# Performance work log

Measured on AMD Instinct MI355X. Metric: run time of the kernel, lower is better.

The kernel has to match this reference:

```python
import jax, jax.numpy as jnp
import numpy as np

EPS = 1e-8


def _conv3x3(x, w, b):
    # x: [B,Ci,H,W], w: [Co,Ci,3,3], 'SAME' padding (stride 1)
    y = jax.lax.conv_general_dilated(x, w, (1, 1), 'SAME',
        dimension_numbers=('NCHW', 'OIHW', 'NCHW'))
    return y + b[None, :, None, None]


def _box3(x):
    # depthwise 3x3 box-sum with zero padding (uniform-kernel masked conv)
    C = x.shape[1]
    k = jnp.ones((C, 1, 3, 3), x.dtype)
    return jax.lax.conv_general_dilated(x, k, (1, 1), 'SAME',
        dimension_numbers=('NCHW', 'OIHW', 'NCHW'), feature_group_count=C)


def _unfold3(x):
    # stack_channel(1,9,k=3,p=1): x [B,1,H,W] -> 9 shifted copies [B,9,H,W]
    H, W = x.shape[-2:]
    xp = jnp.pad(x, ((0, 0), (0, 0), (1, 1), (1, 1)))
    return jnp.concatenate([xp[:, :, i:i + H, j:j + W]
                            for i in range(3) for j in range(3)], axis=1)


def _entropy(x):
    # generate_entropy: sigmoid(neighbor - center) averaged over the 3x3 patch
    # x: [B,1,H,W] -> [B,H,W]
    return jax.nn.sigmoid(_unfold3(x) - x).mean(axis=1)


def _pwf(x, params):
    # PixelWeightedFusionSoftmax: 1x1-conv + ReLU chain 2C->128->32->8->1
    for w, b in params:
        x = jax.nn.relu(jnp.einsum('oc,bchw->bohw', w, x) + b[None, :, None, None])
    return x


def _forward(bevs, compress_w, compress_b, pwf_params):
    BT, N, C, H, W = bevs.shape
    tg = bevs[:, 0]                                    # ego agent  [BT,C,H,W]
    nb = bevs[:, 1:].reshape(BT * (N - 1), C, H, W)    # neighbors

    # myCompressNet: 64 -> 1 channel
    tg_com = jax.nn.relu(_conv3x3(tg, compress_w, compress_b))   # [BT,1,H,W]
    nb_com = jax.nn.relu(_conv3x3(nb, compress_w, compress_b))   # [BT*(N-1),1,H,W]

    tg_ent = _entropy(tg_com)                                    # [BT,H,W]
    nb_ent = _entropy(nb_com).reshape(BT, N - 1, H, W)

    # attention_collaboration: select pixels where neighbor entropy exceeds ego's
    mask = (nb_ent > tg_ent[:, None]).astype(bevs.dtype)         # [BT,N-1,H,W]
    bandwidth = mask.mean()                                      # count / (H*W), averaged

    # conv_mask_uniform / interplot_f: partial conv w/ uniform 3x3 kernel
    m = mask.reshape(BT * (N - 1), 1, H, W)
    num = _box3(nb * m)                                          # [BT*(N-1),C,H,W]
    den = _box3(m)
    inter = num / (den + EPS)
    warp = m * nb + (1.0 - m) * inter

    # all-zero neighbors (min+max==0) are passed through untouched
    is_zero = (nb.min(axis=(1, 2, 3)) + nb.max(axis=(1, 2, 3))) == 0
    warp = jnp.where(is_zero[:, None, None, None], nb, warp)

    feats = jnp.concatenate([tg[:, None], warp.reshape(BT, N - 1, C, H, W)],
                            axis=1)                              # [BT,N,C,H,W]

    # per-agent pixel weights: exp / sum-exp normalize, then weighted fusion
    cat = jnp.concatenate([jnp.broadcast_to(tg[:, None], feats.shape), feats],
                          axis=2)                                # [BT,N,2C,H,W]
    logits = _pwf(cat.reshape(BT * N, 2 * C, H, W), pwf_params)
    logits = logits.reshape(BT, N, 1, H, W)
    wts = jnp.exp(logits)
    wts = wts / wts.sum(axis=1, keepdims=True)
    fused = (wts * feats).sum(axis=1)                            # [BT,C,H,W]
    return fused, bandwidth


def setup_inputs() -> dict:
    key = jax.random.key(0)
    ks = jax.random.split(key, 6)
    BT, N, C, H, W = 3, 5, 64, 200, 200
    s = 0.05
    return {
        'bevs': jax.random.normal(ks[0], (BT, N, C, H, W), jnp.float32),
        'compress_w': jax.random.normal(ks[1], (1, C, 3, 3), jnp.float32) * s,
        'compress_b': jnp.zeros((1,), jnp.float32),
        'pwf_w1': jax.random.normal(ks[2], (128, 2 * C), jnp.float32) * s,
        'pwf_b1': jnp.zeros((128,), jnp.float32),
        'pwf_w2': jax.random.normal(ks[3], (32, 128), jnp.float32) * s,
        'pwf_b2': jnp.zeros((32,), jnp.float32),
        'pwf_w3': jax.random.normal(ks[4], (8, 32), jnp.float32) * s,
        'pwf_b3': jnp.zeros((8,), jnp.float32),
        'pwf_w4': jax.random.normal(ks[5], (1, 8), jnp.float32) * s,
        'pwf_b4': jnp.zeros((1,), jnp.float32),
    }


def reference(bevs, compress_w, compress_b, pwf_w1, pwf_b1, pwf_w2, pwf_b2,
              pwf_w3, pwf_b3, pwf_w4, pwf_b4):
    pwf = [(pwf_w1, pwf_b1), (pwf_w2, pwf_b2), (pwf_w3, pwf_b3), (pwf_w4, pwf_b4)]
    return _forward(bevs, compress_w, compress_b, pwf)
```

## Files before the change

kernel.cpp:

```cpp
#include <hip/hip_runtime.h>
#include <hip/hip_bf16.h>
#include <math.h>

#define PP 40000
#define HDIM 200
#define WDIM 200
#define NEPS 1e-8f
#define GX 157
#define NPART (GX*12)

#define OFF_COM    0
#define OFF_ENT    (15*PP)
#define OFF_MASK   (30*PP)
#define OFF_DEN    (42*PP)
#define OFF_LOGITS (54*PP)
#define OFF_MISC   (69*PP)
#define OFF_XTG_F  (69*PP + 64)
#define OFF_XFT_F  (OFF_XTG_F + 3*PP*32)
#define OFF_WBF_F  (OFF_XFT_F + 12*PP*32)
#define OFF_CNT_F  (OFF_WBF_F + 10240)
#define WS_NEED ((size_t)(OFF_CNT_F + NPART + 64)*4)

typedef __attribute__((ext_vector_type(8))) short bf16x8;
typedef __attribute__((ext_vector_type(4))) float f32x4;

__device__ __forceinline__ short f2bf(float f){
    __hip_bfloat16 h = __float2bfloat16(f);
    return *reinterpret_cast<short*>(&h);
}
__device__ __forceinline__ float bf2f(short s){
    return __uint_as_float(((unsigned)(unsigned short)s) << 16);
}

__device__ __forceinline__ unsigned f2ord(float f){
    unsigned u = __float_as_uint(f);
    return (u & 0x80000000u) ? ~u : (u | 0x80000000u);
}
__device__ __forceinline__ float ord2f(unsigned u){
    unsigned v = (u & 0x80000000u) ? (u & 0x7fffffffu) : ~u;
    return __uint_as_float(v);
}

__device__ __forceinline__ void tap_setup(int p, int* off, bool* val){
    int h = p / WDIM, w = p - h*WDIM;
#pragma unroll
    for (int ky=0;ky<3;ky++)
#pragma unroll
        for (int kx=0;kx<3;kx++){
            int t = ky*3+kx;
            int hh = h+ky-1, ww = w+kx-1;
            val[t] = (hh>=0)&&(hh<HDIM)&&(ww>=0)&&(ww<WDIM);
            int hc = min(max(hh,0),HDIM-1);
            int wc = min(max(ww,0),WDIM-1);
            off[t] = hc*WDIM+wc;
        }
}

__global__ void k_init(unsigned* misc){
    int t = threadIdx.x;
    if (t < 12) misc[t] = 0xFFFFFFFFu;
    else if (t < 25) misc[t] = 0u;
}

__global__ __launch_bounds__(256) void k_wcvt(const float* __restrict__ w1,
        const float* __restrict__ w2, short* __restrict__ wbf)
{
    int i = blockIdx.x*256 + threadIdx.x;
    if (i < 16384){
        int e = i&7, l = (i>>3)&63, ks = (i>>9)&3, nt = i>>11;
        int ln = l&15, kg = l>>4;
        wbf[i] = f2bf(w1[(nt*16+ln)*128 + ks*32 + kg*8 + e]);
    } else if (i < 20480){
        int j = i - 16384;
        int e = j&7, l = (j>>3)&63, ks = (j>>9)&3, nt2 = j>>11;
        int ln = l&15, kg = l>>4;
        wbf[i] = f2bf(w2[(nt2*16+ln)*128 + ks*32 + kg*8 + e]);
    }
}

__global__ __launch_bounds__(256) void k_csum(const float* __restrict__ bevs,
        const float* __restrict__ cw, unsigned* __restrict__ misc,
        float* __restrict__ z)
{
    int img = blockIdx.y;
    int n = img % 5;
    int idx = blockIdx.x*256 + threadIdx.x;
    bool act = idx < PP/4;
    int p = idx*4;
    float vmin = INFINITY, vmax = -INFINITY;
    f32x4 acc[9];
#pragma unroll
    for (int t=0;t<9;t++) acc[t] = (f32x4){0.f,0.f,0.f,0.f};
    if (act){
        const float* src = bevs + (size_t)img*64*PP;
#pragma unroll 2
        for (int c=0;c<64;c++){
            f32x4 v = *(const f32x4*)&src[(size_t)c*PP + p];
            vmin = fminf(fminf(fminf(vmin, v[0]), fminf(v[1], v[2])), v[3]);
            vmax = fmaxf(fmaxf(fmaxf(vmax, v[0]), fmaxf(v[1], v[2])), v[3]);
#pragma unroll
            for (int t=0;t<9;t++){
                float w = cw[c*9+t];
#pragma unroll
                for (int j=0;j<4;j++) acc[t][j] = fmaf(w, v[j], acc[t][j]);
            }
        }
        float* zimg = z + (size_t)img*9*PP;
#pragma unroll
        for (int t=0;t<9;t++)
            *(f32x4*)&zimg[(size_t)t*PP + p] = acc[t];
    }
    if (n > 0){
#pragma unroll
        for (int s=32;s>0;s>>=1){
            vmin = fminf(vmin, __shfl_xor(vmin, s, 64));
            vmax = fmaxf(vmax, __shfl_xor(vmax, s, 64));
        }
        if ((threadIdx.x & 63) == 0){
            int im12 = (img/5)*4 + (n-1);
            atomicMin(&misc[im12], f2ord(vmin));
            atomicMax(&misc[12+im12], f2ord(vmax));
        }
    }
}

__global__ __launch_bounds__(256) void k_cfin(const float* __restrict__ z,
        const float* __restrict__ cb, float* __restrict__ com)
{
    int img = blockIdx.y;
    int p = blockIdx.x*256 + threadIdx.x;
    if (p >= PP) return;
    int off[9]; bool val[9];
    tap_setup(p, off, val);
    const float* zimg = z + (size_t)img*9*PP;
    float v[9];
#pragma unroll
    for (int t=0;t<9;t++) v[t] = zimg[(size_t)t*PP + off[t]];
    float acc = cb[0];
#pragma unroll
    for (int t=0;t<9;t++) acc += val[t] ? v[t] : 0.0f;
    com[(size_t)img*PP + p] = fmaxf(acc, 0.0f);
}

__global__ __launch_bounds__(256) void k_conv(const float* __restrict__ bevs,
        const float* __restrict__ cw, const float* __restrict__ cb,
        float* __restrict__ com, unsigned* __restrict__ misc)
{
    int img = blockIdx.y;
    int n = img % 5;
    int p = blockIdx.x*256 + threadIdx.x;
    float vmin = INFINITY, vmax = -INFINITY;
    if (p < PP){
        int off[9]; bool val[9];
        tap_setup(p, off, val);
        const float* src = bevs + (size_t)img*64*PP;
        float acc = cb[0];
#pragma unroll 2
        for (int c=0;c<64;c++){
            const float* sc = src + (size_t)c*PP;
            float v[9];
#pragma unroll
            for (int t=0;t<9;t++) v[t] = sc[off[t]];
            vmin = fminf(vmin, v[4]); vmax = fmaxf(vmax, v[4]);
#pragma unroll
            for (int t=0;t<9;t++)
                acc = fmaf(cw[c*9+t], val[t] ? v[t] : 0.0f, acc);
        }
        com[(size_t)img*PP + p] = fmaxf(acc, 0.0f);
    }
    if (n > 0){
#pragma unroll
        for (int s=32;s>0;s>>=1){
            vmin = fminf(vmin, __shfl_xor(vmin, s, 64));
            vmax = fmaxf(vmax, __shfl_xor(vmax, s, 64));
        }
        if ((threadIdx.x & 63) == 0){
            int im12 = (img/5)*4 + (n-1);
            atomicMin(&misc[im12], f2ord(vmin));
            atomicMax(&misc[12+im12], f2ord(vmax));
        }
    }
}

__global__ __launch_bounds__(256) void k_ent(const float* __restrict__ com,
        float* __restrict__ ent)
{
    int img = blockIdx.y;
    int p = blockIdx.x*256 + threadIdx.x;
    if (p >= PP) return;
    int off[9]; bool val[9];
    tap_setup(p, off, val);
    const float* s = com + (size_t)img*PP;
    float x = s[p];
    float v[9];
#pragma unroll
    for (int t=0;t<9;t++) v[t] = s[off[t]];
    float acc = 0.0f;
#pragma unroll
    for (int t=0;t<9;t++){
        float xv = val[t] ? v[t] : 0.0f;
        acc += 1.0f/(1.0f + expf(x - xv));
    }
    ent[(size_t)img*PP + p] = acc / 9.0f;
}

__global__ __launch_bounds__(256) void k_maskp(const float* __restrict__ ent,
        float* __restrict__ maskb, unsigned* __restrict__ partial)
{
    __shared__ unsigned cnt[4];
    int im12 = blockIdx.y; int bt = im12 >> 2; int n = (im12 & 3) + 1;
    int p = blockIdx.x*256 + threadIdx.x;
    int v = 0;
    if (p < PP){
        float en = ent[(size_t)(bt*5+n)*PP + p];
        float et = ent[(size_t)(bt*5)*PP + p];
        v = en > et;
        maskb[(size_t)im12*PP + p] = (float)v;
    }
    unsigned long long bal = __ballot(v);
    if ((threadIdx.x & 63) == 0) cnt[threadIdx.x>>6] = (unsigned)__popcll(bal);
    __syncthreads();
    if (threadIdx.x == 0)
        partial[blockIdx.y*GX + blockIdx.x] = cnt[0]+cnt[1]+cnt[2]+cnt[3];
}

__global__ __launch_bounds__(256) void k_mask(const float* __restrict__ ent,
        float* __restrict__ maskb, unsigned* __restrict__ misc)
{
    int im12 = blockIdx.y; int bt = im12 >> 2; int n = (im12 & 3) + 1;
    int p = blockIdx.x*256 + threadIdx.x;
    int v = 0;
    if (p < PP){
        float en = ent[(size_t)(bt*5+n)*PP + p];
        float et = ent[(size_t)(bt*5)*PP + p];
        v = en > et;
        maskb[(size_t)im12*PP + p] = (float)v;
    }
    unsigned long long bal = __ballot(v);
    if ((threadIdx.x & 63) == 0) atomicAdd(&misc[24], (unsigned)__popcll(bal));
}

__global__ __launch_bounds__(256) void k_den(const float* __restrict__ maskb,
        float* __restrict__ denb)
{
    int im12 = blockIdx.y;
    int p = blockIdx.x*256 + threadIdx.x;
    if (p >= PP) return;
    int off[9]; bool val[9];
    tap_setup(p, off, val);
    const float* mrow = maskb + (size_t)im12*PP;
    float v[9];
#pragma unroll
    for (int t=0;t<9;t++) v[t] = mrow[off[t]];
    float s = 0.0f;
#pragma unroll
    for (int t=0;t<9;t++) s += val[t] ? v[t] : 0.0f;
    denb[(size_t)im12*PP + p] = s;
}

__global__ __launch_bounds__(256) void k_finp(const unsigned* __restrict__ partial,
        unsigned* misc, float* bwout)
{
    __shared__ unsigned sh[4];
    unsigned s = 0;
    for (int i = threadIdx.x; i < NPART; i += 256) s += partial[i];
#pragma unroll
    for (int sft=32;sft>0;sft>>=1) s += (unsigned)__shfl_xor((int)s, sft, 64);
    if ((threadIdx.x & 63) == 0) sh[threadIdx.x>>6] = s;
    __syncthreads();
    int t = threadIdx.x;
    if (t < 12){
        float mn = ord2f(misc[t]);
        float mx = ord2f(misc[12+t]);
        ((int*)misc)[25+t] = (mn + mx == 0.0f) ? 1 : 0;
    }
    if (t == 12) bwout[0] = (float)(sh[0]+sh[1]+sh[2]+sh[3]) / 480000.0f;
}

__global__ void k_fin(unsigned* misc, float* bwout){
    int t = threadIdx.x;
    if (t < 12){
        float mn = ord2f(misc[t]);
        float mx = ord2f(misc[12+t]);
        ((int*)misc)[25+t] = (mn + mx == 0.0f) ? 1 : 0;
    }
    if (t == 12) bwout[0] = (float)misc[24] / 480000.0f;
}

__global__ __launch_bounds__(256) void k_xtg(const float* __restrict__ bevs,
        short* __restrict__ Xtg)
{
    __shared__ short tile[64][72];
    int tid = threadIdx.x;
    int bt = blockIdx.y;
    int px0 = blockIdx.x*64;
    const float* tg = bevs + (size_t)bt*5*64*PP;
    int c = tid>>2, q = tid&3;
#pragma unroll
    for (int j=0;j<4;j++){
        int pxl = q*16 + j*4;
        f32x4 v = *(const f32x4*)&tg[(size_t)c*PP + px0 + pxl];
#pragma unroll
        for (int e=0;e<4;e++) tile[pxl+e][c] = f2bf(v[e]);
    }
    __syncthreads();
    int pxl = tid&63, qq = tid>>6;
    short* base = Xtg + (size_t)bt*PP*64;
    *(bf16x8*)&base[((size_t)(2*qq  )*PP + px0 + pxl)*8] = *(bf16x8*)&tile[pxl][qq*16];
    *(bf16x8*)&base[((size_t)(2*qq+1)*PP + px0 + pxl)*8] = *(bf16x8*)&tile[pxl][qq*16+8];
}

__global__ __launch_bounds__(256) void k_xft(const float* __restrict__ bevs,
        const float* __restrict__ maskb, const float* __restrict__ denb,
        const unsigned* __restrict__ misc, short* __restrict__ Xft)
{
    int im12 = blockIdx.y; int bt = im12 >> 2; int n = (im12 & 3) + 1;
    int chunk = blockIdx.z;
    int chb = chunk*8;
    int idx = blockIdx.x*256 + threadIdx.x;
    if (idx >= PP/4) return;
    int p = idx*4;
    int row = p / WDIM, col0 = p - row*WDIM;
    int s0 = max(col0-4, 0), s2 = min(col0+4, WDIM-4);
    int rowc[3]; bool rowok[3];
#pragma unroll
    for (int r=0;r<3;r++){
        int rr = row + r - 1;
        rowok[r] = (rr>=0) && (rr<HDIM);
        rowc[r] = min(max(rr,0),HDIM-1) * WDIM;
    }
    bool colok[6];
#pragma unroll
    for (int k=0;k<6;k++){
        int cc = col0 + k - 1;
        colok[k] = (cc>=0) && (cc<WDIM);
    }
    const float* mrow = maskb + (size_t)im12*PP;
    float m6[3][6];
#pragma unroll
    for (int r=0;r<3;r++){
        f32x4 a0 = *(const f32x4*)&mrow[rowc[r] + s0];
        f32x4 a1 = *(const f32x4*)&mrow[rowc[r] + col0];
        f32x4 a2 = *(const f32x4*)&mrow[rowc[r] + s2];
        float mv[6] = {a0[3], a1[0], a1[1], a1[2], a1[3], a2[0]};
#pragma unroll
        for (int k=0;k<6;k++)
            m6[r][k] = (rowok[r] && colok[k]) ? mv[k] : 0.0f;
    }
    f32x4 den4 = *(const f32x4*)&denb[(size_t)im12*PP + p];
    float rden[4];
#pragma unroll
    for (int j=0;j<4;j++) rden[j] = 1.0f/(den4[j] + NEPS);
    int iz = ((const int*)misc)[25+im12];
    const float* nbb = bevs + (size_t)(bt*5+n)*64*PP;

    short fv0[8], fv1[8], fv2[8], fv3[8];
#pragma unroll
    for (int ci=0;ci<8;ci++){
        int c = chb + ci;
        const float* sc = nbb + (size_t)c*PP;
        f32x4 v0[3], v1[3], v2[3];
#pragma unroll
        for (int r=0;r<3;r++){
            v0[r] = *(const f32x4*)&sc[rowc[r] + s0];
            v1[r] = *(const f32x4*)&sc[rowc[r] + col0];
            v2[r] = *(const f32x4*)&sc[rowc[r] + s2];
        }
        float num[4];
#pragma unroll
        for (int j=0;j<4;j++) num[j] = 0.0f;
#pragma unroll
        for (int r=0;r<3;r++){
            float vv[6] = {v0[r][3], v1[r][0], v1[r][1], v1[r][2], v1[r][3], v2[r][0]};
#pragma unroll
            for (int j=0;j<4;j++){
#pragma unroll
                for (int dk=0;dk<3;dk++)
                    num[j] = fmaf(m6[r][j+dk], vv[j+dk], num[j]);
            }
        }
        short out4[4];
#pragma unroll
        for (int j=0;j<4;j++){
            float center = v1[1][j];
            float mc = m6[1][j+1];
            float xc = iz ? center : fmaf(mc, center, (1.0f-mc)*(num[j]*rden[j]));
            out4[j] = f2bf(xc);
        }
        fv0[ci]=out4[0]; fv1[ci]=out4[1]; fv2[ci]=out4[2]; fv3[ci]=out4[3];
    }
    short* xc0 = Xft + (size_t)im12*PP*64 + ((size_t)chunk*PP + p)*8;
    *(bf16x8*)&xc0[0]  = *(bf16x8*)&fv0[0];
    *(bf16x8*)&xc0[8]  = *(bf16x8*)&fv1[0];
    *(bf16x8*)&xc0[16] = *(bf16x8*)&fv2[0];
    *(bf16x8*)&xc0[24] = *(bf16x8*)&fv3[0];
}

__global__ __launch_bounds__(256) void k_mlp(const short* __restrict__ Xtg,
        const short* __restrict__ Xft, const short* __restrict__ wbf,
        const float* __restrict__ b1, const float* __restrict__ b2,
        const float* __restrict__ w3, const float* __restrict__ b3,
        const float* __restrict__ w4, const float* __restrict__ b4,
        float* __restrict__ logits)
{
    __shared__ __align__(16) short w1t[16384];
    __shared__ __align__(16) short xt2[4*16*136];
    __shared__ __align__(16) float z2[4*16*33];
    __shared__ float b1l[128], b2l[32], b3l[8], w3l[8*33], w4l[8], b4l[1];

    int tid = threadIdx.x;
    int img = blockIdx.y, bt = img/5, n = img%5;

#pragma unroll
    for (int k=0;k<8;k++){
        int i = tid + k*256;
        *(bf16x8*)&w1t[i*8] = *(const bf16x8*)&wbf[i*8];
    }
    if (tid<256) w3l[(tid>>5)*33 + (tid&31)] = w3[tid];
    if (tid<128) b1l[tid]=b1[tid];
    if (tid<32)  b2l[tid]=b2[tid];
    if (tid<8)   b3l[tid]=b3[tid];
    if (tid<8)   w4l[tid]=w4[tid];
    if (tid==0)  b4l[0]=b4[0];

    int w = tid>>6, l = tid&63;
    int ln = l&15, kg = l>>4;

    bf16x8 w2f[2][4];
#pragma unroll
    for (int nt2=0;nt2<2;nt2++)
#pragma unroll
    for (int ks=0;ks<4;ks++)
        w2f[nt2][ks] = *(const bf16x8*)&wbf[16384 + ((nt2*4+ks)*64 + l)*8];

    __syncthreads();

    const short* xtgb = Xtg + (size_t)bt*PP*64;
    const short* xftb = (n>0) ? (Xft + (size_t)(bt*4+n-1)*PP*64) : xtgb;
    short* xt2w = &xt2[w*16*136];
    float* z2w  = &z2[w*16*33];
    int px_base = blockIdx.x*256 + w*64;

#pragma unroll 1
    for (int mt=0; mt<4; mt++){
        int prow = px_base + mt*16;
        int arow = prow + ln; if (arow > PP-1) arow = PP-1;
        bf16x8 af[4];
        af[0] = *(const bf16x8*)&xtgb[((size_t)kg*PP     + arow)*8];
        af[1] = *(const bf16x8*)&xtgb[((size_t)(kg+4)*PP + arow)*8];
        af[2] = *(const bf16x8*)&xftb[((size_t)kg*PP     + arow)*8];
        af[3] = *(const bf16x8*)&xftb[((size_t)(kg+4)*PP + arow)*8];

#pragma unroll
        for (int nt=0;nt<8;nt++){
            float bias = b1l[nt*16 + ln];
            f32x4 acc = {bias, bias, bias, bias};
#pragma unroll
            for (int ks=0;ks<4;ks++){
                bf16x8 bf = *(const bf16x8*)&w1t[((nt*4+ks)*64 + l)*8];
                acc = __builtin_amdgcn_mfma_f32_16x16x32_bf16(af[ks], bf, acc, 0, 0, 0);
            }
#pragma unroll
            for (int r=0;r<4;r++)
                xt2w[(kg*4+r)*136 + nt*16 + ln] = f2bf(fmaxf(acc[r], 0.0f));
        }

        bf16x8 a2[4];
#pragma unroll
        for (int ks=0;ks<4;ks++)
            a2[ks] = *(const bf16x8*)&xt2w[ln*136 + ks*32 + kg*8];
#pragma unroll
        for (int nt2=0;nt2<2;nt2++){
            float bias = b2l[nt2*16 + ln];
            f32x4 acc = {bias, bias, bias, bias};
#pragma unroll
            for (int ks=0;ks<4;ks++)
                acc = __builtin_amdgcn_mfma_f32_16x16x32_bf16(a2[ks], w2f[nt2][ks], acc, 0, 0, 0);
#pragma unroll
            for (int r=0;r<4;r++)
                z2w[(kg*4+r)*33 + nt2*16 + ln] = fmaxf(acc[r], 0.0f);
        }

        int k0 = kg*2, k1 = kg*2+1;
        float y0 = b3l[k0], y1 = b3l[k1];
#pragma unroll
        for (int j=0;j<32;j++){
            float v = z2w[ln*33 + j];
            y0 = fmaf(w3l[k0*33+j], v, y0);
            y1 = fmaf(w3l[k1*33+j], v, y1);
        }
        float part = w4l[k0]*fmaxf(y0,0.0f) + w4l[k1]*fmaxf(y1,0.0f);
        part += __shfl_xor(part, 16, 64);
        part += __shfl_xor(part, 32, 64);
        if (kg == 0 && prow + ln < PP)
            logits[(size_t)img*PP + prow + ln] = fmaxf(part + b4l[0], 0.0f);
    }
}

__global__ __launch_bounds__(256) void k_fuse2(const float* __restrict__ bevs,
        const float* __restrict__ logits, const short* __restrict__ Xft,
        float* __restrict__ out)
{
    int bt = blockIdx.y;
    int cb = blockIdx.z*32;
    int chunk0 = cb>>3;
    int p = blockIdx.x*256 + threadIdx.x;
    if (p >= PP) return;
    float e[5], ssum = 0.0f;
#pragma unroll
    for (int nn=0;nn<5;nn++){ e[nn] = expf(logits[(size_t)(bt*5+nn)*PP + p]); ssum += e[nn]; }
    float rs = 1.0f/ssum;
    const float* tgb = bevs + (size_t)bt*5*64*PP;
    float acc[32];
    float w0 = e[0]*rs;
#pragma unroll
    for (int ci=0;ci<32;ci++) acc[ci] = w0*tgb[(size_t)(cb+ci)*PP + p];
#pragma unroll
    for (int k=0;k<4;k++){
        float wk = e[k+1]*rs;
        const short* Xim = Xft + (size_t)(bt*4+k)*PP*64;
#pragma unroll
        for (int c8=0;c8<4;c8++){
            bf16x8 v = *(const bf16x8*)&Xim[((size_t)(chunk0+c8)*PP + p)*8];
#pragma unroll
            for (int j=0;j<8;j++)
                acc[c8*8+j] = fmaf(wk, bf2f(v[j]), acc[c8*8+j]);
        }
    }
#pragma unroll
    for (int ci=0;ci<32;ci++)
        out[((size_t)bt*64 + cb+ci)*PP + p] = acc[ci];
}

__global__ __launch_bounds__(256) void k_pwf(const float* __restrict__ bevs,
        const float* __restrict__ w1, const float* __restrict__ b1,
        const float* __restrict__ w2, const float* __restrict__ b2,
        const float* __restrict__ w3, const float* __restrict__ b3,
        const float* __restrict__ w4, const float* __restrict__ b4,
        const float* __restrict__ maskb, const float* __restrict__ denb,
        const unsigned* __restrict__ misc, float* __restrict__ logits)
{
    __shared__ __align__(16) short w1t[128*136];
    __shared__ __align__(16) short w2t[32*136];
    __shared__ __align__(16) short xt[64*136];
    __shared__ __align__(16) float z2[64*33];
    __shared__ float b1l[128], b2l[32], b3l[8], w3l[256], w4l[8], b4l[1];

    int tid = threadIdx.x;
    int img = blockIdx.y, bt = img/5, n = img%5;

    for (int i=tid;i<16384;i+=256) w1t[(i>>7)*136 + (i&127)] = f2bf(w1[i]);
    for (int i=tid;i<4096;i+=256)  w2t[(i>>7)*136 + (i&127)] = f2bf(w2[i]);
    if (tid<128) b1l[tid]=b1[tid];
    if (tid<32)  b2l[tid]=b2[tid];
    if (tid<8)   b3l[tid]=b3[tid];
    if (tid<256) w3l[tid]=w3[tid];
    if (tid<8)   w4l[tid]=w4[tid];
    if (tid==0)  b4l[0]=b4[0];

    int px = tid&63, q = tid>>6;
    int p = blockIdx.x*64 + px;
    const float* tg = bevs + (size_t)bt*5*64*PP;
    if (n == 0){
#pragma unroll
        for (int ci=0;ci<16;ci++){
            int c = q*16+ci;
            short v = f2bf(tg[(size_t)c*PP + p]);
            xt[px*136 + c] = v;
            xt[px*136 + 64 + c] = v;
        }
    } else {
        int im12 = bt*4 + (n-1);
        int off[9]; bool val[9];
        tap_setup(p, off, val);
        const float* mrow = maskb + (size_t)im12*PP;
        float m9[9];
#pragma unroll
        for (int t=0;t<9;t++) m9[t] = val[t] ? mrow[off[t]] : 0.0f;
        float rden = 1.0f/(denb[(size_t)im12*PP + p] + NEPS);
        int iz = ((const int*)misc)[25+im12];
        float mc = m9[4];
        const float* nbb = bevs + (size_t)(bt*5+n)*64*PP;
#pragma unroll
        for (int ci=0;ci<16;ci++){
            int c = q*16+ci;
            xt[px*136 + c] = f2bf(tg[(size_t)c*PP + p]);
            const float* sc = nbb + (size_t)c*PP;
            float num = 0.0f, center = 0.0f;
#pragma unroll
            for (int t=0;t<9;t++){
                if (val[t]){
                    float v = sc[off[t]];
                    num = fmaf(m9[t], v, num);
                    if (t==4) center = v;
                }
            }
            float xc = iz ? center : fmaf(mc, center, (1.0f-mc)*(num*rden));
            xt[px*136 + 64 + c] = f2bf(xc);
        }
    }
    __syncthreads();

    int w = tid>>6, l = tid&63;
    int ln = l&15, kg = l>>4;
    bf16x8 af[4];
#pragma unroll
    for (int ks=0;ks<4;ks++)
        af[ks] = *(const bf16x8*)&xt[(w*16+ln)*136 + ks*32 + kg*8];
#pragma unroll
    for (int nt=0;nt<8;nt++){
        float bias = b1l[nt*16 + ln];
        f32x4 acc = {bias, bias, bias, bias};
#pragma unroll
        for (int ks=0;ks<4;ks++){
            bf16x8 bf = *(const bf16x8*)&w1t[(nt*16+ln)*136 + ks*32 + kg*8];
            acc = __builtin_amdgcn_mfma_f32_16x16x32_bf16(af[ks], bf, acc, 0, 0, 0);
        }
#pragma unroll
        for (int r=0;r<4;r++){
            int pr = w*16 + kg*4 + r;
            xt[pr*136 + nt*16 + ln] = f2bf(fmaxf(acc[r], 0.0f));
        }
    }
    bf16x8 a2[4];
#pragma unroll
    for (int ks=0;ks<4;ks++)
        a2[ks] = *(const bf16x8*)&xt[(w*16+ln)*136 + ks*32 + kg*8];
#pragma unroll
    for (int nt2=0;nt2<2;nt2++){
        float bias = b2l[nt2*16 + ln];
        f32x4 acc = {bias, bias, bias, bias};
#pragma unroll
        for (int ks=0;ks<4;ks++){
            bf16x8 bf = *(const bf16x8*)&w2t[(nt2*16+ln)*136 + ks*32 + kg*8];
            acc = __builtin_amdgcn_mfma_f32_16x16x32_bf16(a2[ks], bf, acc, 0, 0, 0);
        }
#pragma unroll
        for (int r=0;r<4;r++){
            int pr = w*16 + kg*4 + r;
            z2[pr*33 + nt2*16 + ln] = fmaxf(acc[r], 0.0f);
        }
    }
    __syncthreads();
    if (tid < 64){
        float y3[8];
#pragma unroll
        for (int k=0;k<8;k++) y3[k] = b3l[k];
        for (int j=0;j<32;j++){
            float v = z2[tid*33 + j];
#pragma unroll
            for (int k=0;k<8;k++) y3[k] = fmaf(w3l[k*32+j], v, y3[k]);
        }
        float sres = b4l[0];
#pragma unroll
        for (int k=0;k<8;k++) sres = fmaf(w4l[k], fmaxf(y3[k], 0.0f), sres);
        logits[(size_t)img*PP + blockIdx.x*64 + tid] = fmaxf(sres, 0.0f);
    }
}

__global__ __launch_bounds__(256) void k_fuse_old(const float* __restrict__ bevs,
        const float* __restrict__ logits, const float* __restrict__ maskb,
        const float* __restrict__ denb, const unsigned* __restrict__ misc,
        float* __restrict__ out)
{
    int bt = blockIdx.y;
    int p = blockIdx.x*256 + threadIdx.x;
    if (p >= PP) return;
    int off[9]; bool val[9];
    tap_setup(p, off, val);
    float e[5], ssum = 0.0f;
#pragma unroll
    for (int nn=0;nn<5;nn++){ e[nn] = expf(logits[(size_t)(bt*5+nn)*PP + p]); ssum += e[nn]; }
    float wts[5];
#pragma unroll
    for (int nn=0;nn<5;nn++) wts[nn] = e[nn] / ssum;
    float m9[4][9]; float rden[4]; int iz[4];
#pragma unroll
    for (int k=0;k<4;k++){
        int im12 = bt*4 + k;
        const float* mrow = maskb + (size_t)im12*PP;
#pragma unroll
        for (int t=0;t<9;t++) m9[k][t] = val[t] ? mrow[off[t]] : 0.0f;
        rden[k] = 1.0f/(denb[(size_t)im12*PP + p] + NEPS);
        iz[k] = ((const int*)misc)[25+im12];
    }
    const float* base = bevs + (size_t)bt*5*64*PP;
    for (int c=0;c<64;c++){
        float tgc = base[(size_t)c*PP + p];
        float fused = wts[0]*tgc;
#pragma unroll
        for (int k=0;k<4;k++){
            const float* sc = base + (size_t)(k+1)*64*PP + (size_t)c*PP;
            float num = 0.0f, center = 0.0f;
#pragma unroll
            for (int t=0;t<9;t++){
                if (val[t]){
                    float v = sc[off[t]];
                    num = fmaf(m9[k][t], v, num);
                    if (t==4) center = v;
                }
            }
            float mc = m9[k][4];
            float xc = iz[k] ? center : fmaf(mc, center, (1.0f-mc)*(num*rden[k]));
            fused = fmaf(wts[k+1], xc, fused);
        }
        out[((size_t)bt*64 + c)*PP + p] = fused;
    }
}

extern "C" void kernel_launch(void* const* d_in, const int* in_sizes, int n_in,
                              void* d_out, int out_size, void* d_ws, size_t ws_size,
                              hipStream_t stream)
{
    const float* bevs = (const float*)d_in[0];
    const float* cw  = (const float*)d_in[1];
    const float* cb  = (const float*)d_in[2];
    const float* w1  = (const float*)d_in[3];
    const float* b1  = (const float*)d_in[4];
    const float* w2  = (const float*)d_in[5];
    const float* b2  = (const float*)d_in[6];
    const float* w3  = (const float*)d_in[7];
    const float* b3  = (const float*)d_in[8];
    const float* w4  = (const float*)d_in[9];
    const float* b4  = (const float*)d_in[10];
    float* out = (float*)d_out;
    float* ws = (float*)d_ws;

    float* com    = ws + OFF_COM;
    float* ent    = ws + OFF_ENT;
    float* maskb  = ws + OFF_MASK;
    float* denb   = ws + OFF_DEN;
    float* logits = ws + OFF_LOGITS;
    unsigned* misc = (unsigned*)(ws + OFF_MISC);
    short* Xtg    = (short*)(ws + OFF_XTG_F);
    short* Xft    = (short*)(ws + OFF_XFT_F);
    short* wbf    = (short*)(ws + OFF_WBF_F);
    unsigned* cntp = (unsigned*)(ws + OFF_CNT_F);
    float* z      = (float*)(ws + OFF_XFT_F);

    dim3 blk(256,1,1);
    int gx = GX;
    bool big = ws_size >= WS_NEED;

    k_init<<<dim3(1),dim3(64),0,stream>>>(misc);
    if (big){
        k_wcvt<<<dim3(80),blk,0,stream>>>(w1,w2,wbf);
        k_csum<<<dim3((PP/4+255)/256,15),blk,0,stream>>>(bevs,cw,misc,z);
        k_cfin<<<dim3(gx,15),blk,0,stream>>>(z,cb,com);
        k_xtg <<<dim3(PP/64,3),blk,0,stream>>>(bevs,Xtg);
    } else {
        k_conv<<<dim3(gx,15),blk,0,stream>>>(bevs,cw,cb,com,misc);
    }
    k_ent <<<dim3(gx,15),blk,0,stream>>>(com,ent);
    if (big){
        k_maskp<<<dim3(gx,12),blk,0,stream>>>(ent,maskb,cntp);
        k_den <<<dim3(gx,12),blk,0,stream>>>(maskb,denb);
        k_finp<<<dim3(1),blk,0,stream>>>(cntp, misc, out + (size_t)3*64*PP);
        k_xft  <<<dim3((PP/4+255)/256,12,8),blk,0,stream>>>(bevs,maskb,denb,misc,Xft);
        k_mlp  <<<dim3(gx,15),blk,0,stream>>>(Xtg,Xft,wbf,b1,b2,w3,b3,w4,b4,logits);
        k_fuse2<<<dim3(gx,3,2),blk,0,stream>>>(bevs,logits,Xft,out);
    } else {
        k_mask<<<dim3(gx,12),blk,0,stream>>>(ent,maskb,misc);
        k_den <<<dim3(gx,12),blk,0,stream>>>(maskb,denb);
        k_fin <<<dim3(1),dim3(64),0,stream>>>(misc, out + (size_t)3*64*PP);
        k_pwf  <<<dim3(PP/64,15),blk,0,stream>>>(bevs,w1,b1,w2,b2,w3,b3,w4,b4,maskb,denb,misc,logits);
        k_fuse_old<<<dim3(gx,3),blk,0,stream>>>(bevs,logits,maskb,denb,misc,out);
    }
}
```

Before: 250.8 us.

## Fuse mask box-sum into k_xft and share halo columns via wavefront shuffles

Drops the separate k_den launch and computes the 3x3 mask box-sum (denominator) inside k_xft from the mask values it already loads. Replaces the three overlapping vector loads per row (left, center, right) with one center load plus shfl_up/shfl_down to get neighbour columns, using scalar loads only at wavefront edge lanes. Out-of-range threads now stay alive and clamp their index so the shuffles are valid, and the stores are predicated instead. Also adds a min-blocks occupancy hint to launch_bounds, at the cost of extra shuffle instructions and divergent edge-lane loads.

```diff
diff --git a/kernel.cpp b/kernel.cpp
--- a/kernel.cpp
+++ b/kernel.cpp
@@ -310,18 +310,20 @@
     *(bf16x8*)&base[((size_t)(2*qq+1)*PP + px0 + pxl)*8] = *(bf16x8*)&tile[pxl][qq*16+8];
 }
 
-__global__ __launch_bounds__(256) void k_xft(const float* __restrict__ bevs,
-        const float* __restrict__ maskb, const float* __restrict__ denb,
+__global__ __launch_bounds__(256,5) void k_xft(const float* __restrict__ bevs,
+        const float* __restrict__ maskb,
         const unsigned* __restrict__ misc, short* __restrict__ Xft)
 {
     int im12 = blockIdx.y; int bt = im12 >> 2; int n = (im12 & 3) + 1;
     int chunk = blockIdx.z;
     int chb = chunk*8;
     int idx = blockIdx.x*256 + threadIdx.x;
-    if (idx >= PP/4) return;
+    bool act = idx < PP/4;
+    if (!act) idx = PP/4 - 1;
+    int lane = threadIdx.x & 63;
     int p = idx*4;
     int row = p / WDIM, col0 = p - row*WDIM;
-    int s0 = max(col0-4, 0), s2 = min(col0+4, WDIM-4);
+    int cl = max(col0-1, 0), cr = min(col0+4, WDIM-1);
     int rowc[3]; bool rowok[3];
 #pragma unroll
     for (int r=0;r<3;r++){
@@ -336,21 +338,41 @@
         colok[k] = (cc>=0) && (cc<WDIM);
     }
     const float* mrow = maskb + (size_t)im12*PP;
+    f32x4 mcv[3]; float mle[3], mri[3];
+#pragma unroll
+    for (int r=0;r<3;r++) mcv[r] = *(const f32x4*)&mrow[rowc[r] + col0];
+#pragma unroll
+    for (int r=0;r<3;r++){
+        mle[r] = __shfl_up(mcv[r][3], 1, 64);
+        mri[r] = __shfl_down(mcv[r][0], 1, 64);
+    }
+    if (lane == 0){
+#pragma unroll
+        for (int r=0;r<3;r++) mle[r] = mrow[rowc[r] + cl];
+    }
+    if (lane == 63){
+#pragma unroll
+        for (int r=0;r<3;r++) mri[r] = mrow[rowc[r] + cr];
+    }
     float m6[3][6];
 #pragma unroll
     for (int r=0;r<3;r++){
-        f32x4 a0 = *(const f32x4*)&mrow[rowc[r] + s0];
-        f32x4 a1 = *(const f32x4*)&mrow[rowc[r] + col0];
-        f32x4 a2 = *(const f32x4*)&mrow[rowc[r] + s2];
-        float mv[6] = {a0[3], a1[0], a1[1], a1[2], a1[3], a2[0]};
+        float mv[6] = {mle[r], mcv[r][0], mcv[r][1], mcv[r][2], mcv[r][3], mri[r]};
 #pragma unroll
         for (int k=0;k<6;k++)
             m6[r][k] = (rowok[r] && colok[k]) ? mv[k] : 0.0f;
     }
-    f32x4 den4 = *(const f32x4*)&denb[(size_t)im12*PP + p];
     float rden[4];
 #pragma unroll
-    for (int j=0;j<4;j++) rden[j] = 1.0f/(den4[j] + NEPS);
+    for (int j=0;j<4;j++){
+        float d = 0.0f;
+#pragma unroll
+        for (int r=0;r<3;r++){
+#pragma unroll
+            for (int dk=0;dk<3;dk++) d += m6[r][j+dk];
+        }
+        rden[j] = 1.0f/(d + NEPS);
+    }
     int iz = ((const int*)misc)[25+im12];
     const float* nbb = bevs + (size_t)(bt*5+n)*64*PP;
 
@@ -359,19 +381,29 @@
     for (int ci=0;ci<8;ci++){
         int c = chb + ci;
         const float* sc = nbb + (size_t)c*PP;
-        f32x4 v0[3], v1[3], v2[3];
+        f32x4 vc[3];
+#pragma unroll
+        for (int r=0;r<3;r++) vc[r] = *(const f32x4*)&sc[rowc[r] + col0];
+        float le[3], ri[3];
 #pragma unroll
         for (int r=0;r<3;r++){
-            v0[r] = *(const f32x4*)&sc[rowc[r] + s0];
-            v1[r] = *(const f32x4*)&sc[rowc[r] + col0];
-            v2[r] = *(const f32x4*)&sc[rowc[r] + s2];
+            le[r] = __shfl_up(vc[r][3], 1, 64);
+            ri[r] = __shfl_down(vc[r][0], 1, 64);
+        }
+        if (lane == 0){
+#pragma unroll
+            for (int r=0;r<3;r++) le[r] = sc[rowc[r] + cl];
+        }
+        if (lane == 63){
+#pragma unroll
+            for (int r=0;r<3;r++) ri[r] = sc[rowc[r] + cr];
         }
         float num[4];
 #pragma unroll
         for (int j=0;j<4;j++) num[j] = 0.0f;
 #pragma unroll
         for (int r=0;r<3;r++){
-            float vv[6] = {v0[r][3], v1[r][0], v1[r][1], v1[r][2], v1[r][3], v2[r][0]};
+            float vv[6] = {le[r], vc[r][0], vc[r][1], vc[r][2], vc[r][3], ri[r]};
 #pragma unroll
             for (int j=0;j<4;j++){
 #pragma unroll
@@ -382,18 +414,20 @@
         short out4[4];
 #pragma unroll
         for (int j=0;j<4;j++){
-            float center = v1[1][j];
+            float center = vc[1][j];
             float mc = m6[1][j+1];
             float xc = iz ? center : fmaf(mc, center, (1.0f-mc)*(num[j]*rden[j]));
             out4[j] = f2bf(xc);
         }
         fv0[ci]=out4[0]; fv1[ci]=out4[1]; fv2[ci]=out4[2]; fv3[ci]=out4[3];
     }
-    short* xc0 = Xft + (size_t)im12*PP*64 + ((size_t)chunk*PP + p)*8;
-    *(bf16x8*)&xc0[0]  = *(bf16x8*)&fv0[0];
-    *(bf16x8*)&xc0[8]  = *(bf16x8*)&fv1[0];
-    *(bf16x8*)&xc0[16] = *(bf16x8*)&fv2[0];
-    *(bf16x8*)&xc0[24] = *(bf16x8*)&fv3[0];
+    if (act){
+        short* xc0 = Xft + (size_t)im12*PP*64 + ((size_t)chunk*PP + p)*8;
+        *(bf16x8*)&xc0[0]  = *(bf16x8*)&fv0[0];
+        *(bf16x8*)&xc0[8]  = *(bf16x8*)&fv1[0];
+        *(bf16x8*)&xc0[16] = *(bf16x8*)&fv2[0];
+        *(bf16x8*)&xc0[24] = *(bf16x8*)&fv3[0];
+    }
 }
 
 __global__ __launch_bounds__(256) void k_mlp(const short* __restrict__ Xtg,
@@ -754,9 +788,8 @@
     k_ent <<<dim3(gx,15),blk,0,stream>>>(com,ent);
     if (big){
         k_maskp<<<dim3(gx,12),blk,0,stream>>>(ent,maskb,cntp);
-        k_den <<<dim3(gx,12),blk,0,stream>>>(maskb,denb);
         k_finp<<<dim3(1),blk,0,stream>>>(cntp, misc, out + (size_t)3*64*PP);
-        k_xft  <<<dim3((PP/4+255)/256,12,8),blk,0,stream>>>(bevs,maskb,denb,misc,Xft);
+        k_xft  <<<dim3((PP/4+255)/256,12,8),blk,0,stream>>>(bevs,maskb,misc,Xft);
         k_mlp  <<<dim3(gx,15),blk,0,stream>>>(Xtg,Xft,wbf,b1,b2,w3,b3,w4,b4,logits);
         k_fuse2<<<dim3(gx,3,2),blk,0,stream>>>(bevs,logits,Xft,out);
     } else {
```

Measured after the change: 353.8 us (median of 2 runs). 1.41x slower.
